# Kernel optimization log

Hardware: AMD Instinct MI355X
Metric: run time of the kernel (lower is better)

The kernel has to match this reference:

```python
import jax, jax.numpy as jnp
import numpy as np

NEG_INF = -1e9  # finite stand-in for -inf masked_fill (safe under softmax)


def setup_inputs() -> dict:
    B, T, S, D = 64, 128, 1024, 1024
    key = jax.random.key(0)
    k1, k2, k3, k4, k5, k6 = jax.random.split(key, 6)
    source = jax.random.normal(k1, (B, T, D), dtype=jnp.float32)
    memory_bank = jax.random.normal(k2, (B, S, D), dtype=jnp.float32)
    probs = jax.random.uniform(k3, (B, S), dtype=jnp.float32)
    # lengths in [S//2, S] so every row has valid positions
    memory_lengths = jax.random.randint(k4, (B,), S // 2, S + 1)
    scale = 1.0 / np.sqrt(D)
    W_in = jax.random.normal(k5, (D, D), dtype=jnp.float32) * scale   # linear_in.weight
    W_out = jax.random.normal(k6, (D, 2 * D), dtype=jnp.float32) * scale  # linear_out.weight (no bias)
    return {"source": source, "memory_bank": memory_bank, "probs": probs,
            "memory_lengths": memory_lengths, "W_in": W_in, "W_out": W_out}


def reference(source, memory_bank, probs, memory_lengths, W_in, W_out):
    B, T, D = source.shape
    S = memory_bank.shape[1]
    # score (general): (source @ W_in^T) @ memory_bank^T -> [B, T, S]
    q = jnp.einsum('btd,ed->bte', source, W_in)
    align = jnp.einsum('bte,bse->bts', q, memory_bank)
    # length mask [B, 1, S]
    mask = (jnp.arange(S)[None, :] < memory_lengths[:, None])[:, None, :]
    align = jnp.where(mask, align, NEG_INF)
    # softmax before rescale
    norescale_av = jax.nn.softmax(align, axis=-1)                 # [B, T, S]
    # rescale by key probabilities, re-mask, renormalize
    scaled = norescale_av * probs[:, None, :]
    scaled = scaled * mask.astype(scaled.dtype)
    align_vectors = scaled / jnp.sum(scaled, axis=-1, keepdims=True)
    # context
    c = jnp.einsum('bts,bsd->btd', align_vectors, memory_bank)    # [B, T, D]
    # concat + linear_out + tanh
    concat_c = jnp.concatenate([c, source], axis=-1)              # [B, T, 2D]
    attn_h = jnp.tanh(jnp.einsum('btf,df->btd', concat_c, W_out))
    # outputs are [tgt_len, batch, ...]
    return (attn_h.transpose(1, 0, 2),
            align_vectors.transpose(1, 0, 2),
            norescale_av.transpose(1, 0, 2))
```

## Files before the change

### kernel.cpp

```cpp
#include <hip/hip_runtime.h>
#include <cmath>

constexpr int Bn = 64;
constexpr int Tn = 128;
constexpr int Sn = 1024;
constexpr int Dn = 1024;

typedef __attribute__((ext_vector_type(8))) _Float16 half8;
typedef __attribute__((ext_vector_type(4))) _Float16 half4;
typedef __attribute__((ext_vector_type(4))) float float4v;

__device__ __forceinline__ void split2(float x, _Float16& h, _Float16& l) {
  h = (_Float16)x;
  l = (_Float16)(x - (float)h);
}


__device__ __forceinline__ void stageT_split(const float* __restrict__ G, size_t ld,
                                             int row0, int k0,
                                             _Float16 (*Sh)[40], _Float16 (*Sl)[40],
                                             int tid) {
#pragma unroll
  for (int it = 0; it < 4; ++it) {
    const int f = tid + it * 256;
    const int r = f >> 3, kq = (f & 7) << 2;
    const float4 v = *reinterpret_cast<const float4*>(G + (size_t)(row0 + r) * ld + k0 + kq);
    _Float16 h0, h1, h2, h3, l0, l1, l2, l3;
    split2(v.x, h0, l0); split2(v.y, h1, l1); split2(v.z, h2, l2); split2(v.w, h3, l3);
    half4 hv = {h0, h1, h2, h3};
    half4 lv = {l0, l1, l2, l3};
    *reinterpret_cast<half4*>(&Sh[r][kq]) = hv;
    *reinterpret_cast<half4*>(&Sl[r][kq]) = lv;
  }
}

__device__ __forceinline__ void stageT_split64(const float* __restrict__ G, size_t ld,
                                               int row0, int k0,
                                               _Float16 (*Sh)[40], _Float16 (*Sl)[40],
                                               int tid) {
#pragma unroll
  for (int it = 0; it < 2; ++it) {
    const int f = tid + it * 256;
    const int r = f >> 3, kq = (f & 7) << 2;
    const float4 v = *reinterpret_cast<const float4*>(G + (size_t)(row0 + r) * ld + k0 + kq);
    _Float16 h0, h1, h2, h3, l0, l1, l2, l3;
    split2(v.x, h0, l0); split2(v.y, h1, l1); split2(v.z, h2, l2); split2(v.w, h3, l3);
    half4 hv = {h0, h1, h2, h3};
    half4 lv = {l0, l1, l2, l3};
    *reinterpret_cast<half4*>(&Sh[r][kq]) = hv;
    *reinterpret_cast<half4*>(&Sl[r][kq]) = lv;
  }
}

__device__ __forceinline__ void stageT_plain(const float* __restrict__ G, size_t ld,
                                             int row0, int k0,
                                             _Float16 (*Sh)[40], int tid) {
#pragma unroll
  for (int it = 0; it < 4; ++it) {
    const int f = tid + it * 256;
    const int r = f >> 3, kq = (f & 7) << 2;
    const float4 v = *reinterpret_cast<const float4*>(G + (size_t)(row0 + r) * ld + k0 + kq);
    half4 hv = {(_Float16)v.x, (_Float16)v.y, (_Float16)v.z, (_Float16)v.w};
    *reinterpret_cast<half4*>(&Sh[r][kq]) = hv;
  }
}

__device__ __forceinline__ void stageT_h16(const _Float16* __restrict__ Gh,
                                           const _Float16* __restrict__ Gl, size_t ld,
                                           int row0, int k0,
                                           _Float16 (*Sh)[40], _Float16 (*Sl)[40],
                                           int tid) {
#pragma unroll
  for (int it = 0; it < 2; ++it) {
    const int f = tid + it * 256;
    const int r = f >> 2, kq = (f & 3) << 3;
    *reinterpret_cast<half8*>(&Sh[r][kq]) =
        *reinterpret_cast<const half8*>(Gh + (size_t)(row0 + r) * ld + k0 + kq);
    *reinterpret_cast<half8*>(&Sl[r][kq]) =
        *reinterpret_cast<const half8*>(Gl + (size_t)(row0 + r) * ld + k0 + kq);
  }
}

__device__ __forceinline__ void stageN_plain(const float* __restrict__ G, size_t ld,
                                             int k0, int col0,
                                             _Float16 (*Sk)[136], int tid) {
#pragma unroll
  for (int it = 0; it < 4; ++it) {
    const int f = tid + it * 256;
    const int k = f >> 5, n0 = (f & 31) << 2;
    const float4 v = *reinterpret_cast<const float4*>(G + (size_t)(k0 + k) * ld + col0 + n0);
    half4 hv = {(_Float16)v.x, (_Float16)v.y, (_Float16)v.z, (_Float16)v.w};
    *reinterpret_cast<half4*>(&Sk[k][n0]) = hv;
  }
}


__device__ __forceinline__ void mma_split3(const _Float16 (*Ah)[40], const _Float16 (*Al)[40],
                                           const _Float16 (*Bh)[40], const _Float16 (*Bl)[40],
                                           float4v acc[4][4], int lane, int wr, int wc) {
  const int g = lane >> 4, rr = lane & 15, kb = g << 3;
  half8 ah[4], al[4];
#pragma unroll
  for (int m = 0; m < 4; ++m) {
    ah[m] = *reinterpret_cast<const half8*>(&Ah[wr * 64 + m * 16 + rr][kb]);
    al[m] = *reinterpret_cast<const half8*>(&Al[wr * 64 + m * 16 + rr][kb]);
  }
#pragma unroll
  for (int n = 0; n < 4; ++n) {
    const half8 bh = *reinterpret_cast<const half8*>(&Bh[wc * 64 + n * 16 + rr][kb]);
    const half8 bl = *reinterpret_cast<const half8*>(&Bl[wc * 64 + n * 16 + rr][kb]);
#pragma unroll
    for (int m = 0; m < 4; ++m) {
      acc[m][n] = __builtin_amdgcn_mfma_f32_16x16x32_f16(ah[m], bh, acc[m][n], 0, 0, 0);
      acc[m][n] = __builtin_amdgcn_mfma_f32_16x16x32_f16(al[m], bh, acc[m][n], 0, 0, 0);
      acc[m][n] = __builtin_amdgcn_mfma_f32_16x16x32_f16(ah[m], bl, acc[m][n], 0, 0, 0);
    }
  }
}

__device__ __forceinline__ void mma64_split3(const _Float16 (*Ah)[40], const _Float16 (*Al)[40],
                                             const _Float16 (*Bh)[40], const _Float16 (*Bl)[40],
                                             float4v acc[4][2], int lane, int wc) {
  const int g = lane >> 4, rr = lane & 15, kb = g << 3;
  half8 ah[4], al[4];
#pragma unroll
  for (int m = 0; m < 4; ++m) {
    ah[m] = *reinterpret_cast<const half8*>(&Ah[m * 16 + rr][kb]);
    al[m] = *reinterpret_cast<const half8*>(&Al[m * 16 + rr][kb]);
  }
#pragma unroll
  for (int n = 0; n < 2; ++n) {
    const half8 bh = *reinterpret_cast<const half8*>(&Bh[wc * 32 + n * 16 + rr][kb]);
    const half8 bl = *reinterpret_cast<const half8*>(&Bl[wc * 32 + n * 16 + rr][kb]);
#pragma unroll
    for (int m = 0; m < 4; ++m) {
      acc[m][n] = __builtin_amdgcn_mfma_f32_16x16x32_f16(ah[m], bh, acc[m][n], 0, 0, 0);
      acc[m][n] = __builtin_amdgcn_mfma_f32_16x16x32_f16(al[m], bh, acc[m][n], 0, 0, 0);
      acc[m][n] = __builtin_amdgcn_mfma_f32_16x16x32_f16(ah[m], bl, acc[m][n], 0, 0, 0);
    }
  }
}

__device__ __forceinline__ void mma64_split2(const _Float16 (*Ah)[40], const _Float16 (*Al)[40],
                                             const _Float16 (*Bh)[40],
                                             float4v acc[4][2], int lane, int wc) {
  const int g = lane >> 4, rr = lane & 15, kb = g << 3;
  half8 ah[4], al[4];
#pragma unroll
  for (int m = 0; m < 4; ++m) {
    ah[m] = *reinterpret_cast<const half8*>(&Ah[m * 16 + rr][kb]);
    al[m] = *reinterpret_cast<const half8*>(&Al[m * 16 + rr][kb]);
  }
#pragma unroll
  for (int n = 0; n < 2; ++n) {
    const half8 b = *reinterpret_cast<const half8*>(&Bh[wc * 32 + n * 16 + rr][kb]);
#pragma unroll
    for (int m = 0; m < 4; ++m) {
      acc[m][n] = __builtin_amdgcn_mfma_f32_16x16x32_f16(ah[m], b, acc[m][n], 0, 0, 0);
      acc[m][n] = __builtin_amdgcn_mfma_f32_16x16x32_f16(al[m], b, acc[m][n], 0, 0, 0);
    }
  }
}

__device__ __forceinline__ void mma_gatherB(const _Float16 (*Ah)[40], const _Float16 (*Bk)[136],
                                            float4v acc[4][4], int lane, int wr, int wc) {
  const int g = lane >> 4, rr = lane & 15, kb = g << 3;
  half8 ah[4];
#pragma unroll
  for (int m = 0; m < 4; ++m)
    ah[m] = *reinterpret_cast<const half8*>(&Ah[wr * 64 + m * 16 + rr][kb]);
#pragma unroll
  for (int n = 0; n < 4; ++n) {
    const int nc = wc * 64 + n * 16 + rr;
    half8 b;
#pragma unroll
    for (int j = 0; j < 8; ++j) b[j] = Bk[kb + j][nc];
#pragma unroll
    for (int m = 0; m < 4; ++m)
      acc[m][n] = __builtin_amdgcn_mfma_f32_16x16x32_f16(ah[m], b, acc[m][n], 0, 0, 0);
  }
}

__global__ void __launch_bounds__(256) g1_k(const float* __restrict__ src,
                                            const float* __restrict__ Win,
                                            _Float16* __restrict__ qh,
                                            _Float16* __restrict__ ql) {
  __shared__ _Float16 Ah[64][40], Al[64][40], Bh[128][40], Bl[128][40];
  const int tid = threadIdx.x, lane = tid & 63, wc = tid >> 6;
  const int f = blockIdx.y * 8 + blockIdx.x;
  const int w = (f & 7) * 128 + (f >> 3);
  const int row0 = (w >> 3) * 64, col0 = (w & 7) * 128;
  float4v acc[4][2] = {};
  for (int k0 = 0; k0 < Dn; k0 += 32) {
    stageT_split64(src, Dn, row0, k0, Ah, Al, tid);
    stageT_split(Win, Dn, col0, k0, Bh, Bl, tid);
    __syncthreads();
    mma64_split3(Ah, Al, Bh, Bl, acc, lane, wc);
    __syncthreads();
  }
  const int g = lane >> 4, rr = lane & 15;
#pragma unroll
  for (int m = 0; m < 4; ++m)
#pragma unroll
    for (int n = 0; n < 2; ++n)
#pragma unroll
      for (int i = 0; i < 4; ++i) {
        const int row = row0 + m * 16 + g * 4 + i;
        const int col = col0 + wc * 32 + n * 16 + rr;
        _Float16 h, l; split2(acc[m][n][i], h, l);
        qh[(size_t)row * Dn + col] = h;
        ql[(size_t)row * Dn + col] = l;
      }
}

__global__ void __launch_bounds__(256) g2_k(const _Float16* __restrict__ qh,
                                            const _Float16* __restrict__ ql,
                                            const float* __restrict__ mb,
                                            float* __restrict__ out1) {
  __shared__ _Float16 Ah[128][40], Al[128][40], Bh[128][40], Bl[128][40];
  const int tid = threadIdx.x, lane = tid & 63, wv = tid >> 6;
  const int wr = wv >> 1, wc = wv & 1;
  const int f = blockIdx.z * 8 + blockIdx.x;
  const int w = (f & 7) * 64 + (f >> 3);
  const int b = w >> 3, col0 = (w & 7) * 128;
  const _Float16* qhb = qh + (size_t)b * Tn * Dn;
  const _Float16* qlb = ql + (size_t)b * Tn * Dn;
  const float* mbb = mb + (size_t)b * Sn * Dn;
  float* Cb = out1 + (size_t)b * Sn;
  float4v acc[4][4] = {};
  for (int k0 = 0; k0 < Dn; k0 += 32) {
    stageT_h16(qhb, qlb, Dn, 0, k0, Ah, Al, tid);
    stageT_split(mbb, Dn, col0, k0, Bh, Bl, tid);
    __syncthreads();
    mma_split3(Ah, Al, Bh, Bl, acc, lane, wr, wc);
    __syncthreads();
  }
  const int g = lane >> 4, rr = lane & 15;
#pragma unroll
  for (int m = 0; m < 4; ++m)
#pragma unroll
    for (int n = 0; n < 4; ++n)
#pragma unroll
      for (int i = 0; i < 4; ++i) {
        const int t = wr * 64 + m * 16 + g * 4 + i;
        const int s = col0 + wc * 64 + n * 16 + rr;
        Cb[(size_t)t * (Bn * Sn) + s] = acc[m][n][i];
      }
}

__device__ __forceinline__ float block_max(float v, float* red, int tid) {
#pragma unroll
  for (int o = 32; o; o >>= 1) v = fmaxf(v, __shfl_xor(v, o));
  if ((tid & 63) == 0) red[tid >> 6] = v;
  __syncthreads();
  v = fmaxf(fmaxf(red[0], red[1]), fmaxf(red[2], red[3]));
  __syncthreads();
  return v;
}

__device__ __forceinline__ float block_sum(float v, float* red, int tid) {
#pragma unroll
  for (int o = 32; o; o >>= 1) v += __shfl_xor(v, o);
  if ((tid & 63) == 0) red[tid >> 6] = v;
  __syncthreads();
  v = red[0] + red[1] + red[2] + red[3];
  __syncthreads();
  return v;
}

__global__ void __launch_bounds__(256) softmax_k(float* __restrict__ av_io,
                                                 const float* __restrict__ probs,
                                                 const int* __restrict__ lens,
                                                 float* __restrict__ out_nore) {
  __shared__ float red[4];
  const int r = blockIdx.x;
  const int b = r & (Bn - 1);
  const int tid = threadIdx.x;
  const int len = lens[b];
  float* row = av_io + (size_t)r * Sn;
  const int s0 = tid * 4;

  const float4 x = *reinterpret_cast<const float4*>(row + s0);
  const bool v0 = (s0 + 0) < len, v1 = (s0 + 1) < len, v2 = (s0 + 2) < len, v3 = (s0 + 3) < len;

  float lm = -1e30f;
  if (v0) lm = fmaxf(lm, x.x);
  if (v1) lm = fmaxf(lm, x.y);
  if (v2) lm = fmaxf(lm, x.z);
  if (v3) lm = fmaxf(lm, x.w);
  const float m = block_max(lm, red, tid);

  const float e0 = v0 ? __expf(x.x - m) : 0.f;
  const float e1 = v1 ? __expf(x.y - m) : 0.f;
  const float e2 = v2 ? __expf(x.z - m) : 0.f;
  const float e3 = v3 ? __expf(x.w - m) : 0.f;
  const float esum = block_sum(e0 + e1 + e2 + e3, red, tid);
  const float rs = 1.f / esum;
  const float n0 = e0 * rs, n1 = e1 * rs, n2 = e2 * rs, n3 = e3 * rs;
  *reinterpret_cast<float4*>(out_nore + (size_t)r * Sn + s0) = make_float4(n0, n1, n2, n3);

  const float4 p = *reinterpret_cast<const float4*>(probs + (size_t)b * Sn + s0);
  const float c0 = n0 * p.x, c1 = n1 * p.y, c2 = n2 * p.z, c3 = n3 * p.w;
  const float ssum = block_sum(c0 + c1 + c2 + c3, red, tid);
  const float rss = 1.f / ssum;
  *reinterpret_cast<float4*>(row + s0) = make_float4(c0 * rss, c1 * rss, c2 * rss, c3 * rss);
}

__global__ void __launch_bounds__(256) g4_k(const float* __restrict__ av,
                                            const float* __restrict__ mb,
                                            float* __restrict__ c) {
  __shared__ _Float16 Ah[128][40];
  __shared__ _Float16 Bk[32][136];
  const int tid = threadIdx.x, lane = tid & 63, wv = tid >> 6;
  const int wr = wv >> 1, wc = wv & 1;
  const int f = blockIdx.z * 8 + blockIdx.x;
  const int w = (f & 7) * 64 + (f >> 3);
  const int b = w >> 3, col0 = (w & 7) * 128;
  const float* avb = av + (size_t)b * Sn;
  const float* mbb = mb + (size_t)b * Sn * Dn;
  float* cb = c + (size_t)b * Tn * Dn;
  float4v acc[4][4] = {};
  for (int k0 = 0; k0 < Sn; k0 += 32) {
    stageT_plain(avb, (size_t)Bn * Sn, 0, k0, Ah, tid);
    stageN_plain(mbb, Dn, k0, col0, Bk, tid);
    __syncthreads();
    mma_gatherB(Ah, Bk, acc, lane, wr, wc);
    __syncthreads();
  }
  const int g = lane >> 4, rr = lane & 15;
#pragma unroll
  for (int m = 0; m < 4; ++m)
#pragma unroll
    for (int n = 0; n < 4; ++n)
#pragma unroll
      for (int i = 0; i < 4; ++i) {
        const int t = wr * 64 + m * 16 + g * 4 + i;
        const int d = col0 + wc * 64 + n * 16 + rr;
        cb[(size_t)t * Dn + d] = acc[m][n][i];
      }
}

__global__ void __launch_bounds__(256) g5_k(const float* __restrict__ c,
                                            const float* __restrict__ src,
                                            const float* __restrict__ Wout,
                                            float* __restrict__ out0) {
  __shared__ _Float16 Ah[64][40], Al[64][40], Bh[128][40];
  const int tid = threadIdx.x, lane = tid & 63, wc = tid >> 6;
  const int f = blockIdx.y * 8 + blockIdx.x;
  const int w = (f & 7) * 128 + (f >> 3);
  const int row0 = (w >> 3) * 64, col0 = (w & 7) * 128;
  float4v acc[4][2] = {};
  for (int k0 = 0; k0 < 2 * Dn; k0 += 32) {
    const float* Aop = (k0 < Dn) ? c : src;
    const int ka = k0 & (Dn - 1);
    stageT_split64(Aop, Dn, row0, ka, Ah, Al, tid);
    stageT_plain(Wout, 2 * Dn, col0, k0, Bh, tid);
    __syncthreads();
    mma64_split2(Ah, Al, Bh, acc, lane, wc);
    __syncthreads();
  }
  const int g = lane >> 4, rr = lane & 15;
#pragma unroll
  for (int m = 0; m < 4; ++m)
#pragma unroll
    for (int n = 0; n < 2; ++n)
#pragma unroll
      for (int i = 0; i < 4; ++i) {
        const int mm = row0 + m * 16 + g * 4 + i;
        const int bb = mm >> 7;
        const int t = mm & 127;
        const int d = col0 + wc * 32 + n * 16 + rr;
        out0[((size_t)t * Bn + bb) * Dn + d] = tanhf(acc[m][n][i]);
      }
}


extern "C" void kernel_launch(void* const* d_in, const int* in_sizes, int n_in,
                              void* d_out, int out_size, void* d_ws, size_t ws_size,
                              hipStream_t stream) {
  const float* src   = (const float*)d_in[0];
  const float* mb    = (const float*)d_in[1];
  const float* probs = (const float*)d_in[2];
  const int*   lens  = (const int*)d_in[3];
  const float* Win   = (const float*)d_in[4];
  const float* Wout  = (const float*)d_in[5];

  float* out  = (float*)d_out;
  float* out0 = out;
  float* out1 = out + (size_t)Tn * Bn * Dn;
  float* out2 = out1 + (size_t)Tn * Bn * Sn;

  _Float16* qh = (_Float16*)d_ws;
  _Float16* ql = qh + (size_t)Bn * Tn * Dn;
  float* cbuf = (float*)d_ws;

  g1_k<<<dim3(Dn / 128, (Bn * Tn) / 64), 256, 0, stream>>>(src, Win, qh, ql);

  g2_k<<<dim3(Sn / 128, 1, Bn), 256, 0, stream>>>(qh, ql, mb, out1);

  softmax_k<<<Tn * Bn, 256, 0, stream>>>(out1, probs, lens, out2);

  g4_k<<<dim3(Dn / 128, 1, Bn), 256, 0, stream>>>(out1, mb, cbuf);

  g5_k<<<dim3(Dn / 128, (Bn * Tn) / 64), 256, 0, stream>>>(cbuf, src, Wout, out0);
}
```

Before: 349.1 us.

## Halve g2 tile width, store context as fp16, drop split precision in output GEMM

```diff
diff --git a/kernel.cpp b/kernel.cpp
--- a/kernel.cpp
+++ b/kernel.cpp
@@ -81,6 +81,45 @@
   }
 }
 
+
+__device__ __forceinline__ void stage64x64_h16(const _Float16* __restrict__ G, size_t ld,
+                                               int row0, int k0,
+                                               _Float16 (*Sh)[72], int tid) {
+#pragma unroll
+  for (int it = 0; it < 2; ++it) {
+    const int f = tid + it * 256;
+    const int r = f >> 3, kq = (f & 7) << 3;
+    *reinterpret_cast<half8*>(&Sh[r][kq]) =
+        *reinterpret_cast<const half8*>(G + (size_t)(row0 + r) * ld + k0 + kq);
+  }
+}
+
+__device__ __forceinline__ void stage64x64_f32(const float* __restrict__ G, size_t ld,
+                                               int row0, int k0,
+                                               _Float16 (*Sh)[72], int tid) {
+#pragma unroll
+  for (int it = 0; it < 4; ++it) {
+    const int f = tid + it * 256;
+    const int r = f >> 4, kq = (f & 15) << 2;
+    const float4 v = *reinterpret_cast<const float4*>(G + (size_t)(row0 + r) * ld + k0 + kq);
+    half4 hv = {(_Float16)v.x, (_Float16)v.y, (_Float16)v.z, (_Float16)v.w};
+    *reinterpret_cast<half4*>(&Sh[r][kq]) = hv;
+  }
+}
+
+__device__ __forceinline__ void stage128x64_f32(const float* __restrict__ G, size_t ld,
+                                                int row0, int k0,
+                                                _Float16 (*Sh)[72], int tid) {
+#pragma unroll
+  for (int it = 0; it < 8; ++it) {
+    const int f = tid + it * 256;
+    const int r = f >> 4, kq = (f & 15) << 2;
+    const float4 v = *reinterpret_cast<const float4*>(G + (size_t)(row0 + r) * ld + k0 + kq);
+    half4 hv = {(_Float16)v.x, (_Float16)v.y, (_Float16)v.z, (_Float16)v.w};
+    *reinterpret_cast<half4*>(&Sh[r][kq]) = hv;
+  }
+}
+
 __device__ __forceinline__ void stageN_plain(const float* __restrict__ G, size_t ld,
                                              int k0, int col0,
                                              _Float16 (*Sk)[136], int tid) {
@@ -95,20 +134,20 @@
 }
 
 
-__device__ __forceinline__ void mma_split3(const _Float16 (*Ah)[40], const _Float16 (*Al)[40],
-                                           const _Float16 (*Bh)[40], const _Float16 (*Bl)[40],
-                                           float4v acc[4][4], int lane, int wr, int wc) {
+__device__ __forceinline__ void mma64_split3(const _Float16 (*Ah)[40], const _Float16 (*Al)[40],
+                                             const _Float16 (*Bh)[40], const _Float16 (*Bl)[40],
+                                             float4v acc[4][2], int lane, int wc) {
   const int g = lane >> 4, rr = lane & 15, kb = g << 3;
   half8 ah[4], al[4];
 #pragma unroll
   for (int m = 0; m < 4; ++m) {
-    ah[m] = *reinterpret_cast<const half8*>(&Ah[wr * 64 + m * 16 + rr][kb]);
-    al[m] = *reinterpret_cast<const half8*>(&Al[wr * 64 + m * 16 + rr][kb]);
-  }
-#pragma unroll
-  for (int n = 0; n < 4; ++n) {
-    const half8 bh = *reinterpret_cast<const half8*>(&Bh[wc * 64 + n * 16 + rr][kb]);
-    const half8 bl = *reinterpret_cast<const half8*>(&Bl[wc * 64 + n * 16 + rr][kb]);
+    ah[m] = *reinterpret_cast<const half8*>(&Ah[m * 16 + rr][kb]);
+    al[m] = *reinterpret_cast<const half8*>(&Al[m * 16 + rr][kb]);
+  }
+#pragma unroll
+  for (int n = 0; n < 2; ++n) {
+    const half8 bh = *reinterpret_cast<const half8*>(&Bh[wc * 32 + n * 16 + rr][kb]);
+    const half8 bl = *reinterpret_cast<const half8*>(&Bl[wc * 32 + n * 16 + rr][kb]);
 #pragma unroll
     for (int m = 0; m < 4; ++m) {
       acc[m][n] = __builtin_amdgcn_mfma_f32_16x16x32_f16(ah[m], bh, acc[m][n], 0, 0, 0);
@@ -118,15 +157,15 @@
   }
 }
 
-__device__ __forceinline__ void mma64_split3(const _Float16 (*Ah)[40], const _Float16 (*Al)[40],
-                                             const _Float16 (*Bh)[40], const _Float16 (*Bl)[40],
-                                             float4v acc[4][2], int lane, int wc) {
+__device__ __forceinline__ void mma12864_split3(const _Float16 (*Ah)[40], const _Float16 (*Al)[40],
+                                                const _Float16 (*Bh)[40], const _Float16 (*Bl)[40],
+                                                float4v acc[4][2], int lane, int wr, int wc) {
   const int g = lane >> 4, rr = lane & 15, kb = g << 3;
   half8 ah[4], al[4];
 #pragma unroll
   for (int m = 0; m < 4; ++m) {
-    ah[m] = *reinterpret_cast<const half8*>(&Ah[m * 16 + rr][kb]);
-    al[m] = *reinterpret_cast<const half8*>(&Al[m * 16 + rr][kb]);
+    ah[m] = *reinterpret_cast<const half8*>(&Ah[wr * 64 + m * 16 + rr][kb]);
+    al[m] = *reinterpret_cast<const half8*>(&Al[wr * 64 + m * 16 + rr][kb]);
   }
 #pragma unroll
   for (int n = 0; n < 2; ++n) {
@@ -141,23 +180,22 @@
   }
 }
 
-__device__ __forceinline__ void mma64_split2(const _Float16 (*Ah)[40], const _Float16 (*Al)[40],
-                                             const _Float16 (*Bh)[40],
-                                             float4v acc[4][2], int lane, int wc) {
-  const int g = lane >> 4, rr = lane & 15, kb = g << 3;
-  half8 ah[4], al[4];
-#pragma unroll
-  for (int m = 0; m < 4; ++m) {
-    ah[m] = *reinterpret_cast<const half8*>(&Ah[m * 16 + rr][kb]);
-    al[m] = *reinterpret_cast<const half8*>(&Al[m * 16 + rr][kb]);
-  }
-#pragma unroll
-  for (int n = 0; n < 2; ++n) {
-    const half8 b = *reinterpret_cast<const half8*>(&Bh[wc * 32 + n * 16 + rr][kb]);
-#pragma unroll
-    for (int m = 0; m < 4; ++m) {
-      acc[m][n] = __builtin_amdgcn_mfma_f32_16x16x32_f16(ah[m], b, acc[m][n], 0, 0, 0);
-      acc[m][n] = __builtin_amdgcn_mfma_f32_16x16x32_f16(al[m], b, acc[m][n], 0, 0, 0);
+__device__ __forceinline__ void mma64_bk64_plain(const _Float16 (*Ah)[72], const _Float16 (*Bh)[72],
+                                                 float4v acc[4][2], int lane, int wc) {
+  const int g = lane >> 4, rr = lane & 15;
+#pragma unroll
+  for (int kk = 0; kk < 2; ++kk) {
+    const int kb = kk * 32 + (g << 3);
+    half8 ah[4];
+#pragma unroll
+    for (int m = 0; m < 4; ++m)
+      ah[m] = *reinterpret_cast<const half8*>(&Ah[m * 16 + rr][kb]);
+#pragma unroll
+    for (int n = 0; n < 2; ++n) {
+      const half8 b = *reinterpret_cast<const half8*>(&Bh[wc * 32 + n * 16 + rr][kb]);
+#pragma unroll
+      for (int m = 0; m < 4; ++m)
+        acc[m][n] = __builtin_amdgcn_mfma_f32_16x16x32_f16(ah[m], b, acc[m][n], 0, 0, 0);
     }
   }
 }
@@ -217,33 +255,33 @@
                                             const _Float16* __restrict__ ql,
                                             const float* __restrict__ mb,
                                             float* __restrict__ out1) {
-  __shared__ _Float16 Ah[128][40], Al[128][40], Bh[128][40], Bl[128][40];
+  __shared__ _Float16 Ah[128][40], Al[128][40], Bh[64][40], Bl[64][40];
   const int tid = threadIdx.x, lane = tid & 63, wv = tid >> 6;
   const int wr = wv >> 1, wc = wv & 1;
-  const int f = blockIdx.z * 8 + blockIdx.x;
-  const int w = (f & 7) * 64 + (f >> 3);
-  const int b = w >> 3, col0 = (w & 7) * 128;
+  const int id = blockIdx.z * 16 + blockIdx.x;
+  const int j = id >> 3;
+  const int b = (id & 7) * 8 + (j >> 4), col0 = (j & 15) * 64;
   const _Float16* qhb = qh + (size_t)b * Tn * Dn;
   const _Float16* qlb = ql + (size_t)b * Tn * Dn;
   const float* mbb = mb + (size_t)b * Sn * Dn;
   float* Cb = out1 + (size_t)b * Sn;
-  float4v acc[4][4] = {};
+  float4v acc[4][2] = {};
   for (int k0 = 0; k0 < Dn; k0 += 32) {
     stageT_h16(qhb, qlb, Dn, 0, k0, Ah, Al, tid);
-    stageT_split(mbb, Dn, col0, k0, Bh, Bl, tid);
-    __syncthreads();
-    mma_split3(Ah, Al, Bh, Bl, acc, lane, wr, wc);
+    stageT_split64(mbb, Dn, col0, k0, Bh, Bl, tid);
+    __syncthreads();
+    mma12864_split3(Ah, Al, Bh, Bl, acc, lane, wr, wc);
     __syncthreads();
   }
   const int g = lane >> 4, rr = lane & 15;
 #pragma unroll
   for (int m = 0; m < 4; ++m)
 #pragma unroll
-    for (int n = 0; n < 4; ++n)
+    for (int n = 0; n < 2; ++n)
 #pragma unroll
       for (int i = 0; i < 4; ++i) {
         const int t = wr * 64 + m * 16 + g * 4 + i;
-        const int s = col0 + wc * 64 + n * 16 + rr;
+        const int s = col0 + wc * 32 + n * 16 + rr;
         Cb[(size_t)t * (Bn * Sn) + s] = acc[m][n][i];
       }
 }
@@ -308,17 +346,17 @@
 
 __global__ void __launch_bounds__(256) g4_k(const float* __restrict__ av,
                                             const float* __restrict__ mb,
-                                            float* __restrict__ c) {
+                                            _Float16* __restrict__ c) {
   __shared__ _Float16 Ah[128][40];
   __shared__ _Float16 Bk[32][136];
   const int tid = threadIdx.x, lane = tid & 63, wv = tid >> 6;
   const int wr = wv >> 1, wc = wv & 1;
-  const int f = blockIdx.z * 8 + blockIdx.x;
-  const int w = (f & 7) * 64 + (f >> 3);
-  const int b = w >> 3, col0 = (w & 7) * 128;
+  const int id = blockIdx.z * 8 + blockIdx.x;
+  const int j = id >> 3;
+  const int b = (id & 7) * 8 + (j >> 3), col0 = (j & 7) * 128;
   const float* avb = av + (size_t)b * Sn;
   const float* mbb = mb + (size_t)b * Sn * Dn;
-  float* cb = c + (size_t)b * Tn * Dn;
+  _Float16* cb = c + (size_t)b * Tn * Dn;
   float4v acc[4][4] = {};
   for (int k0 = 0; k0 < Sn; k0 += 32) {
     stageT_plain(avb, (size_t)Bn * Sn, 0, k0, Ah, tid);
@@ -336,27 +374,26 @@
       for (int i = 0; i < 4; ++i) {
         const int t = wr * 64 + m * 16 + g * 4 + i;
         const int d = col0 + wc * 64 + n * 16 + rr;
-        cb[(size_t)t * Dn + d] = acc[m][n][i];
+        cb[(size_t)t * Dn + d] = (_Float16)acc[m][n][i];
       }
 }
 
-__global__ void __launch_bounds__(256) g5_k(const float* __restrict__ c,
+__global__ void __launch_bounds__(256) g5_k(const _Float16* __restrict__ c,
                                             const float* __restrict__ src,
                                             const float* __restrict__ Wout,
                                             float* __restrict__ out0) {
-  __shared__ _Float16 Ah[64][40], Al[64][40], Bh[128][40];
+  __shared__ _Float16 Ah[64][72], Bh[128][72];
   const int tid = threadIdx.x, lane = tid & 63, wc = tid >> 6;
   const int f = blockIdx.y * 8 + blockIdx.x;
   const int w = (f & 7) * 128 + (f >> 3);
   const int row0 = (w >> 3) * 64, col0 = (w & 7) * 128;
   float4v acc[4][2] = {};
-  for (int k0 = 0; k0 < 2 * Dn; k0 += 32) {
-    const float* Aop = (k0 < Dn) ? c : src;
-    const int ka = k0 & (Dn - 1);
-    stageT_split64(Aop, Dn, row0, ka, Ah, Al, tid);
-    stageT_plain(Wout, 2 * Dn, col0, k0, Bh, tid);
-    __syncthreads();
-    mma64_split2(Ah, Al, Bh, acc, lane, wc);
+  for (int k0 = 0; k0 < 2 * Dn; k0 += 64) {
+    if (k0 < Dn) stage64x64_h16(c, Dn, row0, k0, Ah, tid);
+    else         stage64x64_f32(src, Dn, row0, k0 - Dn, Ah, tid);
+    stage128x64_f32(Wout, 2 * Dn, col0, k0, Bh, tid);
+    __syncthreads();
+    mma64_bk64_plain(Ah, Bh, acc, lane, wc);
     __syncthreads();
   }
   const int g = lane >> 4, rr = lane & 15;
@@ -392,11 +429,11 @@
 
   _Float16* qh = (_Float16*)d_ws;
   _Float16* ql = qh + (size_t)Bn * Tn * Dn;
-  float* cbuf = (float*)d_ws;
+  _Float16* cbuf = (_Float16*)d_ws;
 
   g1_k<<<dim3(Dn / 128, (Bn * Tn) / 64), 256, 0, stream>>>(src, Win, qh, ql);
 
-  g2_k<<<dim3(Sn / 128, 1, Bn), 256, 0, stream>>>(qh, ql, mb, out1);
+  g2_k<<<dim3(Sn / 64, 1, Bn), 256, 0, stream>>>(qh, ql, mb, out1);
 
   softmax_k<<<Tn * Bn, 256, 0, stream>>>(out1, probs, lens, out2);
 
```

Result: faster. 339.5 us (-2.8%).
